# Kernel optimization log

Hardware: AMD Instinct MI355X
Metric: run time of the kernel (lower is better)

The kernel has to match this reference:

```python
import jax, jax.numpy as jnp
import numpy as np

B, L, D, N_ITEMS = 512, 100, 128, 100000
ALPHA = 0.3


def setup_inputs() -> dict:
    key = jax.random.key(0)
    ks = jax.random.split(key, 10)
    x = jax.random.randint(ks[0], (B, L), 0, N_ITEMS, dtype=jnp.int32)
    attn_mask = jnp.ones((B, L), dtype=bool)  # unused by forward (parity with torch signature)
    emb = jax.random.normal(ks[1], (N_ITEMS, D), dtype=jnp.float32) * 0.02
    emb = emb.at[0].set(0.0)  # padding_idx=0 row is zeros
    s = 1.0 / np.sqrt(D)
    W_in = jax.random.uniform(ks[2], (D, D), minval=-s, maxval=s, dtype=jnp.float32)
    W_out = jax.random.uniform(ks[3], (D, D), minval=-s, maxval=s, dtype=jnp.float32)
    w_ih = jax.random.uniform(ks[4], (3 * D, D), minval=-s, maxval=s, dtype=jnp.float32)
    w_hh = jax.random.uniform(ks[5], (3 * D, D), minval=-s, maxval=s, dtype=jnp.float32)
    b_ih = jax.random.uniform(ks[6], (3 * D,), minval=-s, maxval=s, dtype=jnp.float32)
    b_hh = jax.random.uniform(ks[7], (3 * D,), minval=-s, maxval=s, dtype=jnp.float32)
    sr = 1.0 / np.sqrt(3 * D)
    W_read = jax.random.uniform(ks[8], (D, 3 * D), minval=-sr, maxval=sr, dtype=jnp.float32)
    b_read = jax.random.uniform(ks[9], (D,), minval=-sr, maxval=sr, dtype=jnp.float32)
    return dict(x=x, attn_mask=attn_mask, emb=emb, W_in=W_in, W_out=W_out,
                w_ih=w_ih, w_hh=w_hh, b_ih=b_ih, b_hh=b_hh, W_read=W_read, b_read=b_read)


def _forward(x, emb, W_in, W_out, w_ih, w_hh, b_ih, b_hh, W_read, b_read):
    n_items, d = emb.shape
    seq_len = x.shape[1]
    BIG = n_items  # sentinel > any item id
    NEG = -1e9

    def per_sample(seq):
        valid = seq != 0
        cnt = valid.sum()
        # --- torch.unique(nonzero, return_inverse=True) via sort + dedup ---
        s = jnp.where(valid, seq, BIG)
        ss = jnp.sort(s)
        prev = jnp.concatenate([jnp.full((1,), -1, ss.dtype), ss[:-1]])
        is_first = (ss != prev) & (ss != BIG)
        n_nodes = is_first.sum()
        rank = jnp.cumsum(is_first) - 1
        nodes_s = jnp.full((seq_len,), BIG, ss.dtype).at[
            jnp.where(is_first, rank, seq_len)].set(ss, mode='drop')  # sorted unique ids, BIG-padded
        node_mask = jnp.arange(seq_len) < n_nodes
        nodes = jnp.where(node_mask, nodes_s, 0)  # pad slots -> item 0 (zero emb row)
        inv = jnp.searchsorted(nodes_s, s)  # inverse indices for valid positions
        # compact nonzero items preserving order (for consecutive-pair edges)
        pos = jnp.cumsum(valid) - 1
        cidx = jnp.where(valid, pos, seq_len)
        compact_inv = jnp.zeros((seq_len,), inv.dtype).at[cidx].set(inv, mode='drop')
        compact_seq = jnp.zeros((seq_len,), seq.dtype).at[cidx].set(seq, mode='drop')
        last_tok = compact_seq[jnp.maximum(cnt - 1, 0)]
        src, dst = compact_inv[:-1], compact_inv[1:]
        edge_mask = jnp.arange(seq_len - 1) < cnt - 1
        # --- message passing: index_add + degree normalize ---
        H0 = emb[nodes]  # [L, d]
        Hin = H0 @ W_in.T
        Hout = H0 @ W_out.T
        dst_safe = jnp.where(edge_mask, dst, seq_len)
        agg = jnp.zeros((seq_len, d), H0.dtype).at[dst_safe].add(
            jnp.where(edge_mask[:, None], Hout[src], 0.0), mode='drop')
        deg = jnp.zeros((seq_len,), H0.dtype).at[dst_safe].add(1.0, mode='drop')
        deg = jnp.maximum(deg, 1.0)
        xin = Hin + agg / deg[:, None]
        # --- GRUCell(xin, H0), torch gate order (r, z, n) ---
        gi = xin @ w_ih.T + b_ih
        gh = H0 @ w_hh.T + b_hh
        gi_r, gi_z, gi_n = jnp.split(gi, 3, axis=-1)
        gh_r, gh_z, gh_n = jnp.split(gh, 3, axis=-1)
        r = jax.nn.sigmoid(gi_r + gh_r)
        z = jax.nn.sigmoid(gi_z + gh_z)
        nct = jnp.tanh(gi_n + r * gh_n)
        H = (1.0 - z) * nct + z * H0
        H = jnp.where(node_mask[:, None], H, 0.0)  # drop padded node slots
        # --- attention readout anchored at last item ---
        li = jnp.clip(jnp.searchsorted(nodes_s, last_tok), 0, seq_len - 1)
        h_last = H[li]
        scores = jnp.where(node_mask, H @ h_last, NEG)
        att = jax.nn.softmax(scores)
        local = att @ H
        gvec = jnp.zeros((d,), H.dtype)  # cooc is None -> zeros_like(local)
        h_read = jnp.tanh(W_read @ jnp.concatenate([h_last, local, ALPHA * gvec]) + b_read)
        row = h_read @ emb.T  # tied output weights
        default = jnp.full((n_items,), NEG, row.dtype).at[0].set(0.0)
        return jnp.where(cnt >= 2, row, default)

    return jax.vmap(per_sample)(x)


def reference(x, attn_mask, emb, W_in, W_out, w_ih, w_hh, b_ih, b_hh, W_read, b_read):
    return _forward(x, emb, W_in, W_out, w_ih, w_hh, b_ih, b_hh, W_read, b_read)
```

## Files before the change

kernel.cpp:

```cpp
#include <hip/hip_runtime.h>
#include <math.h>

#define BATCH 512
#define SEQL  100
#define DIM   128
#define NITEMS 100000
#define NEGV  -1000000000.0f

#define OFF_WREADT 131072
#define OFF_HREAD  180224
#define OFF_DEG    245760
#define OFF_XIN    296960
#define OFF_HOUT   6850560
#define OFF_EPACK_F (OFF_XIN + 131072)
#define OFF_NODES_I 13404160
#define OFF_SRC_I   13455360
#define OFF_DST_I   13506048
#define OFF_INFO_I  13556736
#define OFF_WPACK_F 13558784

typedef __attribute__((ext_vector_type(8))) short bf16x8;
typedef __attribute__((ext_vector_type(4))) short s16x4;
typedef __attribute__((ext_vector_type(4))) float f32x4;

__device__ __forceinline__ unsigned short bf16_rne(float x) {
  unsigned int u = __float_as_uint(x);
  unsigned int r = u + 0x7FFFu + ((u >> 16) & 1u);
  return (unsigned short)(r >> 16);
}
__device__ __forceinline__ float bf16_to_f(unsigned short h) {
  return __uint_as_float(((unsigned int)h) << 16);
}

__global__ void k_prep(const float* __restrict__ w_ih, const float* __restrict__ w_hh,
                       const float* __restrict__ W_in, const float* __restrict__ W_out,
                       const float* __restrict__ W_read, float* __restrict__ ws,
                       unsigned short* __restrict__ wpack) {
  int idx = blockIdx.x * 256 + threadIdx.x;
  if (idx < 98304) {
    int mat = idx / 49152, rem = idx % 49152;
    int n = rem / 128, k = rem % 128;
    float v = (mat ? w_hh : w_ih)[rem];
    unsigned short hi = bf16_rne(v);
    unsigned short lo = bf16_rne(v - bf16_to_f(hi));
    int nt = n >> 4, nn = n & 15, c = k >> 5, quad = (k >> 3) & 3, j = k & 7;
    int lane = quad * 16 + nn;
    size_t base = ((size_t)((mat * 24 + nt) * 4 + c)) * 1024 + (size_t)lane * 8 + j;
    wpack[base] = hi;
    wpack[base + 512] = lo;
  }
  if (idx < 49152) {
    int i = idx / 384, jj = idx % 384;
    ws[OFF_WREADT + jj * 128 + i] = W_read[idx];
  }
  if (idx < 32768) {
    int mat = idx >> 14, rem = idx & 16383;
    int n = rem >> 7, k = rem & 127;
    float v = (mat ? W_out : W_in)[rem];
    unsigned short hi = bf16_rne(v);
    unsigned short lo = bf16_rne(v - bf16_to_f(hi));
    int nt = n >> 4, nn = n & 15, c = k >> 5, quad = (k >> 3) & 3, j = k & 7;
    int lane = quad * 16 + nn;
    size_t base = ((size_t)((mat * 8 + nt) * 4 + c)) * 1024 + (size_t)lane * 8 + j;
    unsigned short* wpack2 = (unsigned short*)ws;
    wpack2[base] = hi;
    wpack2[base + 512] = lo;
  }
}

__global__ void k_build(const int* __restrict__ x, int* __restrict__ nodes,
                        float* __restrict__ deg, int* __restrict__ esrc,
                        int* __restrict__ edst, int* __restrict__ info) {
  int b = blockIdx.x, tid = threadIdx.x;
  __shared__ int sseq[SEQL];
  __shared__ int sfo[SEQL];
  __shared__ unsigned char sisf[SEQL];
  __shared__ int srank[SEQL];
  __shared__ int spos[SEQL];
  __shared__ int scinv[SEQL];
  __shared__ float sdeg[SEQL];
  __shared__ int s_nn, s_cnt;

  if (tid < SEQL) sseq[tid] = x[b * SEQL + tid];
  __syncthreads();
  int t = (tid < SEQL) ? sseq[tid] : 0;
  bool valid = (tid < SEQL) && (t != 0);
  int f = tid;
  if (valid) {
    for (int j = 0; j < tid; ++j) {
      if (sseq[j] == t) { f = j; break; }
    }
  }
  if (tid < SEQL) {
    sfo[tid] = f;
    sisf[tid] = (valid && f == tid) ? 1 : 0;
    sdeg[tid] = 0.f;
  }
  __syncthreads();
  if (tid == 0) {
    int nn = 0, c = 0;
    for (int i = 0; i < SEQL; ++i) {
      srank[i] = nn; nn += sisf[i];
      spos[i] = c;  c += (sseq[i] != 0) ? 1 : 0;
    }
    s_nn = nn; s_cnt = c;
  }
  __syncthreads();
  int nn = s_nn, cnt = s_cnt;
  if (valid) scinv[spos[tid]] = srank[sfo[tid]];
  __syncthreads();
  if (tid < SEQL) {
    if (sisf[tid]) nodes[b * SEQL + srank[tid]] = t;
    if (tid >= nn) nodes[b * SEQL + tid] = 0;
  }
  __syncthreads();
  if (tid == 0) {
    int ec = (cnt >= 2) ? cnt - 1 : 0;
    for (int e = 0; e < ec; ++e) {
      int s = scinv[e], dnode = scinv[e + 1];
      esrc[b * 99 + e] = s;
      edst[b * 99 + e] = dnode;
      sdeg[dnode] += 1.f;
    }
    info[b * 4 + 0] = ec;
    info[b * 4 + 1] = (cnt >= 1) ? scinv[cnt - 1] : 0;
    info[b * 4 + 2] = (cnt >= 2) ? 1 : 0;
    info[b * 4 + 3] = nn;
  }
  __syncthreads();
  if (tid < SEQL) deg[b * SEQL + tid] = fmaxf(sdeg[tid], 1.f);
}

#define GPAD 136
__global__ __launch_bounds__(128) void k_gemm_inout(
    const float* __restrict__ emb, const unsigned short* __restrict__ wpack2,
    const int* __restrict__ nodes, float* __restrict__ xin, float* __restrict__ hout) {
  __shared__ unsigned short Hhi[32 * GPAD];
  __shared__ unsigned short Hlo[32 * GPAD];
  int tid = threadIdx.x;
  int rowbase = blockIdx.x * 32;
  const float4* emb4 = (const float4*)emb;
  for (int e = tid; e < 32 * 32; e += 128) {
    int r = e >> 5, c4 = e & 31;
    int tok = nodes[rowbase + r];
    float4 hv = emb4[(size_t)tok * 32 + c4];
    int base = r * GPAD + c4 * 4;
    float hs[4] = {hv.x, hv.y, hv.z, hv.w};
    #pragma unroll
    for (int q = 0; q < 4; ++q) {
      unsigned short hh = bf16_rne(hs[q]);
      Hhi[base + q] = hh;
      Hlo[base + q] = bf16_rne(hs[q] - bf16_to_f(hh));
    }
  }
  __syncthreads();
  int wave = tid >> 6, lane = tid & 63;
  int quad = lane >> 4, nIdx = lane & 15;
  int mrow = wave * 16 + nIdx;
  bf16x8 aH[4], aL[4];
  #pragma unroll
  for (int c = 0; c < 4; ++c) {
    int off = mrow * GPAD + c * 32 + quad * 8;
    aH[c] = *(const bf16x8*)&Hhi[off];
    aL[c] = *(const bf16x8*)&Hlo[off];
  }
  for (int t = 0; t < 8; ++t) {
    f32x4 accI = (f32x4){0.f, 0.f, 0.f, 0.f};
    f32x4 accO = (f32x4){0.f, 0.f, 0.f, 0.f};
    #pragma unroll
    for (int c = 0; c < 4; ++c) {
      size_t bi = ((size_t)((0 * 8 + t) * 4 + c)) * 1024 + (size_t)lane * 8;
      size_t bo = ((size_t)((1 * 8 + t) * 4 + c)) * 1024 + (size_t)lane * 8;
      bf16x8 BiH = *(const bf16x8*)&wpack2[bi];
      bf16x8 BiL = *(const bf16x8*)&wpack2[bi + 512];
      bf16x8 BoH = *(const bf16x8*)&wpack2[bo];
      bf16x8 BoL = *(const bf16x8*)&wpack2[bo + 512];
      accI = __builtin_amdgcn_mfma_f32_16x16x32_bf16(aH[c], BiH, accI, 0, 0, 0);
      accO = __builtin_amdgcn_mfma_f32_16x16x32_bf16(aH[c], BoH, accO, 0, 0, 0);
      accI = __builtin_amdgcn_mfma_f32_16x16x32_bf16(aL[c], BiH, accI, 0, 0, 0);
      accO = __builtin_amdgcn_mfma_f32_16x16x32_bf16(aL[c], BoH, accO, 0, 0, 0);
      accI = __builtin_amdgcn_mfma_f32_16x16x32_bf16(aH[c], BiL, accI, 0, 0, 0);
      accO = __builtin_amdgcn_mfma_f32_16x16x32_bf16(aH[c], BoL, accO, 0, 0, 0);
    }
    int j = t * 16 + nIdx;
    #pragma unroll
    for (int i = 0; i < 4; ++i) {
      size_t row = (size_t)(rowbase + wave * 16 + quad * 4 + i);
      xin[row * 128 + j]  = accI[i];
      hout[row * 128 + j] = accO[i];
    }
  }
}

__global__ void k_scatter(const float* __restrict__ hout, float* __restrict__ xin,
                          const float* __restrict__ deg, const int* __restrict__ esrc,
                          const int* __restrict__ edst, const int* __restrict__ info) {
  int b = blockIdx.x, k = threadIdx.x;
  __shared__ float agg[SEQL * DIM];
  for (int n = 0; n < SEQL; ++n) agg[n * DIM + k] = 0.f;
  int ec = info[b * 4 + 0];
  for (int e = 0; e < ec; ++e) {
    int s = esrc[b * 99 + e], dn = edst[b * 99 + e];
    agg[dn * DIM + k] += hout[((size_t)(b * SEQL + s)) * DIM + k];
  }
  for (int n = 0; n < SEQL; ++n) {
    float dg = deg[b * SEQL + n];
    size_t idx = ((size_t)(b * SEQL + n)) * DIM + k;
    xin[idx] += agg[n * DIM + k] / dg;
  }
}

__global__ __launch_bounds__(128) void k_gru(
    const float* __restrict__ emb, const int* __restrict__ nodes,
    const unsigned short* __restrict__ wpack, const float* __restrict__ xin,
    const float* __restrict__ b_ih, const float* __restrict__ b_hh,
    const int* __restrict__ info, float* __restrict__ Hbuf) {
  __shared__ unsigned short Xhi[32 * GPAD];
  __shared__ unsigned short Xlo[32 * GPAD];
  __shared__ unsigned short Hhi[32 * GPAD];
  __shared__ unsigned short Hlo[32 * GPAD];
  int tid = threadIdx.x;
  int rowbase = blockIdx.x * 32;
  const float4* emb4 = (const float4*)emb;
  const float4* xin4 = (const float4*)xin;
  for (int e = tid; e < 32 * 32; e += 128) {
    int r = e >> 5, c4 = e & 31;
    int row = rowbase + r;
    float4 xv = xin4[(size_t)row * 32 + c4];
    int tok = nodes[row];
    float4 hv = emb4[(size_t)tok * 32 + c4];
    int base = r * GPAD + c4 * 4;
    float xs[4] = {xv.x, xv.y, xv.z, xv.w};
    float hs[4] = {hv.x, hv.y, hv.z, hv.w};
    #pragma unroll
    for (int q = 0; q < 4; ++q) {
      unsigned short xh = bf16_rne(xs[q]);
      Xhi[base + q] = xh; Xlo[base + q] = bf16_rne(xs[q] - bf16_to_f(xh));
      unsigned short hh = bf16_rne(hs[q]);
      Hhi[base + q] = hh; Hlo[base + q] = bf16_rne(hs[q] - bf16_to_f(hh));
    }
  }
  __syncthreads();
  int wave = tid >> 6, lane = tid & 63;
  int quad = lane >> 4, nIdx = lane & 15;
  int mrow = wave * 16 + nIdx;
  bf16x8 aXh[4], aXl[4], aHh[4], aHl[4];
  #pragma unroll
  for (int c = 0; c < 4; ++c) {
    int off = mrow * GPAD + c * 32 + quad * 8;
    aXh[c] = *(const bf16x8*)&Xhi[off];
    aXl[c] = *(const bf16x8*)&Xlo[off];
    aHh[c] = *(const bf16x8*)&Hhi[off];
    aHl[c] = *(const bf16x8*)&Hlo[off];
  }
  int grows[4]; int zm[4];
  #pragma unroll
  for (int i = 0; i < 4; ++i) {
    int grow = rowbase + wave * 16 + quad * 4 + i;
    grows[i] = grow;
    int bs = grow / SEQL;
    int n = grow - bs * SEQL;
    zm[i] = (n < info[bs * 4 + 3]) ? 1 : 0;
  }

  for (int t = 0; t < 8; ++t) {
    f32x4 acc[3][2];
    #pragma unroll
    for (int g = 0; g < 3; ++g)
      #pragma unroll
      for (int m = 0; m < 2; ++m) acc[g][m] = (f32x4){0.f, 0.f, 0.f, 0.f};

    for (int c = 0; c < 4; ++c) {
      bf16x8 Bh[3][2], Bl[3][2];
      #pragma unroll
      for (int g = 0; g < 3; ++g) {
        int nt = g * 8 + t;
        #pragma unroll
        for (int m = 0; m < 2; ++m) {
          size_t bidx = (size_t)((m * 24 + nt) * 4 + c) * 1024 + (size_t)lane * 8;
          Bh[g][m] = *(const bf16x8*)&wpack[bidx];
          Bl[g][m] = *(const bf16x8*)&wpack[bidx + 512];
        }
      }
      #pragma unroll
      for (int g = 0; g < 3; ++g) {
        acc[g][0] = __builtin_amdgcn_mfma_f32_16x16x32_bf16(aXh[c], Bh[g][0], acc[g][0], 0, 0, 0);
        acc[g][1] = __builtin_amdgcn_mfma_f32_16x16x32_bf16(aHh[c], Bh[g][1], acc[g][1], 0, 0, 0);
      }
      #pragma unroll
      for (int g = 0; g < 3; ++g) {
        acc[g][0] = __builtin_amdgcn_mfma_f32_16x16x32_bf16(aXh[c], Bl[g][0], acc[g][0], 0, 0, 0);
        acc[g][1] = __builtin_amdgcn_mfma_f32_16x16x32_bf16(aHh[c], Bl[g][1], acc[g][1], 0, 0, 0);
      }
      #pragma unroll
      for (int g = 0; g < 3; ++g) {
        acc[g][0] = __builtin_amdgcn_mfma_f32_16x16x32_bf16(aXl[c], Bh[g][0], acc[g][0], 0, 0, 0);
        acc[g][1] = __builtin_amdgcn_mfma_f32_16x16x32_bf16(aHl[c], Bh[g][1], acc[g][1], 0, 0, 0);
      }
    }
    int j = t * 16 + nIdx;
    float biR = b_ih[j],       bhR = b_hh[j];
    float biZ = b_ih[128 + j], bhZ = b_hh[128 + j];
    float biN = b_ih[256 + j], bhN = b_hh[256 + j];
    #pragma unroll
    for (int i = 0; i < 4; ++i) {
      float gr = acc[0][0][i] + biR + acc[0][1][i] + bhR;
      float gz = acc[1][0][i] + biZ + acc[1][1][i] + bhZ;
      float r = 1.f / (1.f + expf(-gr));
      float z = 1.f / (1.f + expf(-gz));
      float nct = tanhf(acc[2][0][i] + biN + r * (acc[2][1][i] + bhN));
      int lrow = wave * 16 + quad * 4 + i;
      float h0 = bf16_to_f(Hhi[lrow * GPAD + j]) + bf16_to_f(Hlo[lrow * GPAD + j]);
      float h = (1.f - z) * nct + z * h0;
      if (!zm[i]) h = 0.f;
      Hbuf[(size_t)grows[i] * 128 + j] = h;
    }
  }
}

#define HLS 129
__global__ void k_attn(const float* __restrict__ Hbuf, const float* __restrict__ ws,
                       const float* __restrict__ b_read, const int* __restrict__ info,
                       float* __restrict__ hread) {
  int b = blockIdx.x, tid = threadIdx.x;
  __shared__ float Hl[SEQL * HLS];
  __shared__ float sc[128];
  __shared__ float hl[128];
  __shared__ float att[SEQL];
  __shared__ float loc[128];
  __shared__ float redm[2], reds[2];
  int nn = info[b * 4 + 3], li = info[b * 4 + 1];
  for (int e = tid; e < SEQL * 128; e += 128) {
    int r = e >> 7, k = e & 127;
    Hl[r * HLS + k] = Hbuf[((size_t)(b * SEQL + r)) * DIM + k];
  }
  __syncthreads();
  hl[tid] = Hl[li * HLS + tid];
  __syncthreads();
  float scr = NEGV;
  if (tid < nn) {
    float s = 0.f;
    for (int k = 0; k < 128; ++k) s += Hl[tid * HLS + k] * hl[k];
    scr = s;
  }
  sc[tid] = scr;
  __syncthreads();
  float m = sc[tid];
  #pragma unroll
  for (int o = 32; o >= 1; o >>= 1) m = fmaxf(m, __shfl_xor(m, o, 64));
  if ((tid & 63) == 0) redm[tid >> 6] = m;
  __syncthreads();
  m = fmaxf(redm[0], redm[1]);
  float e = (tid < SEQL) ? expf(sc[tid] - m) : 0.f;
  float s = e;
  #pragma unroll
  for (int o = 32; o >= 1; o >>= 1) s += __shfl_xor(s, o, 64);
  if ((tid & 63) == 0) reds[tid >> 6] = s;
  __syncthreads();
  float inv = 1.f / (reds[0] + reds[1]);
  if (tid < SEQL) att[tid] = e * inv;
  __syncthreads();
  float lv = 0.f;
  for (int n = 0; n < SEQL; ++n) lv = fmaf(att[n], Hl[n * HLS + tid], lv);
  loc[tid] = lv;
  __syncthreads();
  const float* WrT = ws + OFF_WREADT;
  float acc = b_read[tid];
  for (int j = 0; j < 128; ++j) acc = fmaf(WrT[j * 128 + tid], hl[j], acc);
  for (int j = 0; j < 128; ++j) acc = fmaf(WrT[(128 + j) * 128 + tid], loc[j], acc);
  hread[b * 128 + tid] = tanhf(acc);
}

__global__ __launch_bounds__(256) void k_packA(
    const float* __restrict__ hread, unsigned short* __restrict__ apack) {
  int idx = blockIdx.x * 256 + threadIdx.x;
  if (idx >= 8192) return;
  int lane = idx & 63;
  int kc = (idx >> 6) & 3;
  int mt = idx >> 8;
  int quad = lane >> 4, rr = lane & 15;
  int row = mt * 16 + rr;
  int kbase = kc * 32 + quad * 8;
  const float4* hr4 = (const float4*)(hread + row * 128 + kbase);
  float4 v0 = hr4[0], v1 = hr4[1];
  float vs[8] = {v0.x, v0.y, v0.z, v0.w, v1.x, v1.y, v1.z, v1.w};
  bf16x8 hi, lo;
  #pragma unroll
  for (int j = 0; j < 8; ++j) {
    unsigned short h = bf16_rne(vs[j]);
    hi[j] = (short)h;
    lo[j] = (short)bf16_rne(vs[j] - bf16_to_f(h));
  }
  size_t base = ((size_t)(mt * 4 + kc) * 2) * 512 + (size_t)lane * 8;
  *(bf16x8*)&apack[base] = hi;
  *(bf16x8*)&apack[base + 512] = lo;
}

__global__ __launch_bounds__(256) void k_epack(
    const float* __restrict__ emb, unsigned short* __restrict__ epack) {
  int idx = blockIdx.x * 256 + threadIdx.x;
  int lane = idx & 63;
  int kc = (idx >> 6) & 3;
  int it = idx >> 8;
  int quad = lane >> 4, rr = lane & 15;
  int row = it * 16 + rr;
  int kbase = kc * 32 + quad * 8;
  float4 v0 = {0.f, 0.f, 0.f, 0.f}, v1 = {0.f, 0.f, 0.f, 0.f};
  if (row < NITEMS) {
    const float4* p = (const float4*)(emb + (size_t)row * 128 + kbase);
    v0 = p[0]; v1 = p[1];
  }
  float vs[8] = {v0.x, v0.y, v0.z, v0.w, v1.x, v1.y, v1.z, v1.w};
  bf16x8 hi, lo;
  #pragma unroll
  for (int j = 0; j < 8; ++j) {
    unsigned short h = bf16_rne(vs[j]);
    hi[j] = (short)h;
    lo[j] = (short)bf16_rne(vs[j] - bf16_to_f(h));
  }
  size_t base = ((size_t)(it * 4 + kc) * 2) * 512 + (size_t)lane * 8;
  *(bf16x8*)&epack[base] = hi;
  *(bf16x8*)&epack[base + 512] = lo;
}

__global__ __launch_bounds__(256) void k_out(
    const unsigned short* __restrict__ epack, const unsigned short* __restrict__ apack,
    const int* __restrict__ info, float* __restrict__ out) {
  int tid = threadIdx.x;
  int wave = tid >> 6, lane = tid & 63;
  int quad = lane >> 4, nIdx = lane & 15;
  int b0   = blockIdx.x * 128;
  int itt0 = blockIdx.y * 4;
  int btg0 = blockIdx.x * 8 + wave * 2;

  bf16x8 bh[2][4], bl[2][4];
  #pragma unroll
  for (int m2 = 0; m2 < 2; ++m2)
    #pragma unroll
    for (int kc = 0; kc < 4; ++kc) {
      size_t base = ((size_t)((btg0 + m2) * 4 + kc) * 2) * 512 + (size_t)lane * 8;
      bh[m2][kc] = *(const bf16x8*)&apack[base];
      bl[m2][kc] = *(const bf16x8*)&apack[base + 512];
    }

  f32x4 acc[4][2];
  #pragma unroll
  for (int it = 0; it < 4; ++it)
    #pragma unroll
    for (int m2 = 0; m2 < 2; ++m2) acc[it][m2] = (f32x4){0.f, 0.f, 0.f, 0.f};

  #pragma unroll
  for (int it = 0; it < 4; ++it) {
    #pragma unroll
    for (int kc = 0; kc < 4; ++kc) {
      size_t abase = ((size_t)((itt0 + it) * 4 + kc) * 2) * 512 + (size_t)lane * 8;
      bf16x8 Ah = *(const bf16x8*)&epack[abase];
      bf16x8 Al = *(const bf16x8*)&epack[abase + 512];
      acc[it][0] = __builtin_amdgcn_mfma_f32_16x16x32_bf16(Ah, bh[0][kc], acc[it][0], 0, 0, 0);
      acc[it][1] = __builtin_amdgcn_mfma_f32_16x16x32_bf16(Ah, bh[1][kc], acc[it][1], 0, 0, 0);
      acc[it][0] = __builtin_amdgcn_mfma_f32_16x16x32_bf16(Al, bh[0][kc], acc[it][0], 0, 0, 0);
      acc[it][1] = __builtin_amdgcn_mfma_f32_16x16x32_bf16(Al, bh[1][kc], acc[it][1], 0, 0, 0);
      acc[it][0] = __builtin_amdgcn_mfma_f32_16x16x32_bf16(Ah, bl[0][kc], acc[it][0], 0, 0, 0);
      acc[it][1] = __builtin_amdgcn_mfma_f32_16x16x32_bf16(Ah, bl[1][kc], acc[it][1], 0, 0, 0);
    }
  }

  #pragma unroll
  for (int m2 = 0; m2 < 2; ++m2) {
    int b = b0 + (wave * 2 + m2) * 16 + nIdx;
    int flag = info[b * 4 + 2];
    #pragma unroll
    for (int it = 0; it < 4; ++it) {
      int ib = (itt0 + it) * 16 + quad * 4;
      if (ib < NITEMS) {
        float4 v;
        if (flag) {
          v.x = acc[it][m2][0]; v.y = acc[it][m2][1];
          v.z = acc[it][m2][2]; v.w = acc[it][m2][3];
        } else {
          v.x = (ib == 0) ? 0.f : NEGV; v.y = NEGV; v.z = NEGV; v.w = NEGV;
        }
        *(float4*)&out[(size_t)b * NITEMS + ib] = v;
      }
    }
  }
}

extern "C" void kernel_launch(void* const* d_in, const int* in_sizes, int n_in,
                              void* d_out, int out_size, void* d_ws, size_t ws_size,
                              hipStream_t stream) {
  const int*   x      = (const int*)d_in[0];
  const float* emb    = (const float*)d_in[2];
  const float* W_in   = (const float*)d_in[3];
  const float* W_out  = (const float*)d_in[4];
  const float* w_ih   = (const float*)d_in[5];
  const float* w_hh   = (const float*)d_in[6];
  const float* b_ih   = (const float*)d_in[7];
  const float* b_hh   = (const float*)d_in[8];
  const float* W_read = (const float*)d_in[9];
  const float* b_read = (const float*)d_in[10];
  float* ws  = (float*)d_ws;
  int*   wsi = (int*)d_ws;
  unsigned short* wpack  = (unsigned short*)(ws + OFF_WPACK_F);
  unsigned short* wpack2 = (unsigned short*)ws;
  unsigned short* apack  = (unsigned short*)(ws + OFF_XIN);
  unsigned short* epack  = (unsigned short*)(ws + OFF_EPACK_F);
  float* out = (float*)d_out;

  k_prep<<<384, 256, 0, stream>>>(w_ih, w_hh, W_in, W_out, W_read, ws, wpack);
  k_build<<<BATCH, 128, 0, stream>>>(x, wsi + OFF_NODES_I, ws + OFF_DEG,
                                     wsi + OFF_SRC_I, wsi + OFF_DST_I, wsi + OFF_INFO_I);
  k_gemm_inout<<<1600, 128, 0, stream>>>(emb, wpack2, wsi + OFF_NODES_I,
                                         ws + OFF_XIN, ws + OFF_HOUT);
  k_scatter<<<BATCH, 128, 0, stream>>>(ws + OFF_HOUT, ws + OFF_XIN, ws + OFF_DEG,
                                       wsi + OFF_SRC_I, wsi + OFF_DST_I, wsi + OFF_INFO_I);
  k_gru<<<1600, 128, 0, stream>>>(emb, wsi + OFF_NODES_I, wpack, ws + OFF_XIN,
                                  b_ih, b_hh, wsi + OFF_INFO_I, ws + OFF_HOUT);
  k_attn<<<BATCH, 128, 0, stream>>>(ws + OFF_HOUT, ws, b_read, wsi + OFF_INFO_I,
                                    ws + OFF_HREAD);
  k_epack<<<6252, 256, 0, stream>>>(emb, epack);
  k_packA<<<32, 256, 0, stream>>>(ws + OFF_HREAD, apack);
  k_out<<<dim3(4, 1563), 256, 0, stream>>>(epack, apack, wsi + OFF_INFO_I, out);
}
```

Baseline: 473.5 us.

## Parallelize graph build and scatter, fuse A-packing into attention readout

Replaces the single-thread serial prefix scans and edge loop in k_build with per-thread scans and parallel edge writes, and moves degree counting into k_scatter via shared-memory atomics. k_scatter now uses 256 threads, parallelizes over edges×dims with LDS atomics, and applies the degree normalization in a fused vectorized pass. The separate k_packA launch is removed by having k_attn write the bf16 hi/lo packed output directly. This targets serial latency and launch overhead in the small kernels. The trade-off is float atomic ordering nondeterminism in aggregation and O(n) per-thread scans.

```diff
diff --git a/kernel.cpp b/kernel.cpp
--- a/kernel.cpp
+++ b/kernel.cpp
@@ -8,8 +8,6 @@
 #define NEGV  -1000000000.0f
 
 #define OFF_WREADT 131072
-#define OFF_HREAD  180224
-#define OFF_DEG    245760
 #define OFF_XIN    296960
 #define OFF_HOUT   6850560
 #define OFF_EPACK_F (OFF_XIN + 131072)
@@ -69,66 +67,52 @@
 }
 
 __global__ void k_build(const int* __restrict__ x, int* __restrict__ nodes,
-                        float* __restrict__ deg, int* __restrict__ esrc,
-                        int* __restrict__ edst, int* __restrict__ info) {
+                        int* __restrict__ esrc, int* __restrict__ edst,
+                        int* __restrict__ info) {
   int b = blockIdx.x, tid = threadIdx.x;
   __shared__ int sseq[SEQL];
-  __shared__ int sfo[SEQL];
   __shared__ unsigned char sisf[SEQL];
   __shared__ int srank[SEQL];
-  __shared__ int spos[SEQL];
   __shared__ int scinv[SEQL];
-  __shared__ float sdeg[SEQL];
+  __shared__ int snodes[SEQL];
   __shared__ int s_nn, s_cnt;
-
-  if (tid < SEQL) sseq[tid] = x[b * SEQL + tid];
+  if (tid < SEQL) { sseq[tid] = x[b * SEQL + tid]; snodes[tid] = 0; }
   __syncthreads();
   int t = (tid < SEQL) ? sseq[tid] : 0;
   bool valid = (tid < SEQL) && (t != 0);
   int f = tid;
   if (valid) {
-    for (int j = 0; j < tid; ++j) {
-      if (sseq[j] == t) { f = j; break; }
-    }
-  }
+    for (int j = 0; j < tid; ++j) if (sseq[j] == t) { f = j; break; }
+  }
+  int isf = (valid && f == tid) ? 1 : 0;
+  if (tid < SEQL) sisf[tid] = (unsigned char)isf;
+  __syncthreads();
+  int rank = 0, pos = 0;
   if (tid < SEQL) {
-    sfo[tid] = f;
-    sisf[tid] = (valid && f == tid) ? 1 : 0;
-    sdeg[tid] = 0.f;
-  }
-  __syncthreads();
+    for (int i = 0; i < tid; ++i) {
+      rank += sisf[i];
+      pos += (sseq[i] != 0) ? 1 : 0;
+    }
+    srank[tid] = rank;
+    if (tid == SEQL - 1) { s_nn = rank + isf; s_cnt = pos + (valid ? 1 : 0); }
+  }
+  __syncthreads();
+  if (valid) scinv[pos] = srank[f];
+  if (isf) snodes[rank] = t;
+  __syncthreads();
+  int cnt = s_cnt;
+  int ec = (cnt >= 2) ? cnt - 1 : 0;
+  if (tid < ec) {
+    esrc[b * 99 + tid] = scinv[tid];
+    edst[b * 99 + tid] = scinv[tid + 1];
+  }
   if (tid == 0) {
-    int nn = 0, c = 0;
-    for (int i = 0; i < SEQL; ++i) {
-      srank[i] = nn; nn += sisf[i];
-      spos[i] = c;  c += (sseq[i] != 0) ? 1 : 0;
-    }
-    s_nn = nn; s_cnt = c;
-  }
-  __syncthreads();
-  int nn = s_nn, cnt = s_cnt;
-  if (valid) scinv[spos[tid]] = srank[sfo[tid]];
-  __syncthreads();
-  if (tid < SEQL) {
-    if (sisf[tid]) nodes[b * SEQL + srank[tid]] = t;
-    if (tid >= nn) nodes[b * SEQL + tid] = 0;
-  }
-  __syncthreads();
-  if (tid == 0) {
-    int ec = (cnt >= 2) ? cnt - 1 : 0;
-    for (int e = 0; e < ec; ++e) {
-      int s = scinv[e], dnode = scinv[e + 1];
-      esrc[b * 99 + e] = s;
-      edst[b * 99 + e] = dnode;
-      sdeg[dnode] += 1.f;
-    }
     info[b * 4 + 0] = ec;
     info[b * 4 + 1] = (cnt >= 1) ? scinv[cnt - 1] : 0;
     info[b * 4 + 2] = (cnt >= 2) ? 1 : 0;
-    info[b * 4 + 3] = nn;
-  }
-  __syncthreads();
-  if (tid < SEQL) deg[b * SEQL + tid] = fmaxf(sdeg[tid], 1.f);
+    info[b * 4 + 3] = s_nn;
+  }
+  if (tid < SEQL) nodes[b * SEQL + tid] = snodes[tid];
 }
 
 #define GPAD 136
@@ -192,21 +176,29 @@
   }
 }
 
-__global__ void k_scatter(const float* __restrict__ hout, float* __restrict__ xin,
-                          const float* __restrict__ deg, const int* __restrict__ esrc,
-                          const int* __restrict__ edst, const int* __restrict__ info) {
-  int b = blockIdx.x, k = threadIdx.x;
+__global__ __launch_bounds__(256) void k_scatter(
+    const float* __restrict__ hout, float* __restrict__ xin,
+    const int* __restrict__ esrc, const int* __restrict__ edst,
+    const int* __restrict__ info) {
   __shared__ float agg[SEQL * DIM];
-  for (int n = 0; n < SEQL; ++n) agg[n * DIM + k] = 0.f;
+  __shared__ float sdeg[SEQL];
+  int b = blockIdx.x, tid = threadIdx.x;
+  float4* a4 = (float4*)agg;
+  for (int e = tid; e < SEQL * 32; e += 256) a4[e] = (float4){0.f, 0.f, 0.f, 0.f};
+  if (tid < SEQL) sdeg[tid] = 0.f;
+  __syncthreads();
   int ec = info[b * 4 + 0];
-  for (int e = 0; e < ec; ++e) {
+  if (tid < ec) atomicAdd(&sdeg[edst[b * 99 + tid]], 1.f);
+  for (int idx = tid; idx < ec * DIM; idx += 256) {
+    int e = idx >> 7, k = idx & 127;
     int s = esrc[b * 99 + e], dn = edst[b * 99 + e];
-    agg[dn * DIM + k] += hout[((size_t)(b * SEQL + s)) * DIM + k];
-  }
-  for (int n = 0; n < SEQL; ++n) {
-    float dg = deg[b * SEQL + n];
-    size_t idx = ((size_t)(b * SEQL + n)) * DIM + k;
-    xin[idx] += agg[n * DIM + k] / dg;
+    atomicAdd(&agg[dn * DIM + k], hout[((size_t)(b * SEQL + s)) * DIM + k]);
+  }
+  __syncthreads();
+  for (int idx = tid; idx < SEQL * DIM; idx += 256) {
+    int n = idx >> 7;
+    size_t g = ((size_t)b * SEQL) * DIM + idx;
+    xin[g] += agg[idx] * (1.f / fmaxf(sdeg[n], 1.f));
   }
 }
 
@@ -319,9 +311,9 @@
 }
 
 #define HLS 129
-__global__ void k_attn(const float* __restrict__ Hbuf, const float* __restrict__ ws,
+__global__ void k_attn(const float* __restrict__ Hbuf, const float* __restrict__ WrT,
                        const float* __restrict__ b_read, const int* __restrict__ info,
-                       float* __restrict__ hread) {
+                       unsigned short* __restrict__ apack) {
   int b = blockIdx.x, tid = threadIdx.x;
   __shared__ float Hl[SEQL * HLS];
   __shared__ float sc[128];
@@ -364,36 +356,17 @@
   for (int n = 0; n < SEQL; ++n) lv = fmaf(att[n], Hl[n * HLS + tid], lv);
   loc[tid] = lv;
   __syncthreads();
-  const float* WrT = ws + OFF_WREADT;
   float acc = b_read[tid];
   for (int j = 0; j < 128; ++j) acc = fmaf(WrT[j * 128 + tid], hl[j], acc);
   for (int j = 0; j < 128; ++j) acc = fmaf(WrT[(128 + j) * 128 + tid], loc[j], acc);
-  hread[b * 128 + tid] = tanhf(acc);
-}
-
-__global__ __launch_bounds__(256) void k_packA(
-    const float* __restrict__ hread, unsigned short* __restrict__ apack) {
-  int idx = blockIdx.x * 256 + threadIdx.x;
-  if (idx >= 8192) return;
-  int lane = idx & 63;
-  int kc = (idx >> 6) & 3;
-  int mt = idx >> 8;
-  int quad = lane >> 4, rr = lane & 15;
-  int row = mt * 16 + rr;
-  int kbase = kc * 32 + quad * 8;
-  const float4* hr4 = (const float4*)(hread + row * 128 + kbase);
-  float4 v0 = hr4[0], v1 = hr4[1];
-  float vs[8] = {v0.x, v0.y, v0.z, v0.w, v1.x, v1.y, v1.z, v1.w};
-  bf16x8 hi, lo;
-  #pragma unroll
-  for (int j = 0; j < 8; ++j) {
-    unsigned short h = bf16_rne(vs[j]);
-    hi[j] = (short)h;
-    lo[j] = (short)bf16_rne(vs[j] - bf16_to_f(h));
-  }
-  size_t base = ((size_t)(mt * 4 + kc) * 2) * 512 + (size_t)lane * 8;
-  *(bf16x8*)&apack[base] = hi;
-  *(bf16x8*)&apack[base + 512] = lo;
+  float hr = tanhf(acc);
+  int mt = b >> 4, rr = b & 15;
+  int kc = tid >> 5, q2 = (tid >> 3) & 3, j2 = tid & 7;
+  unsigned short hi = bf16_rne(hr);
+  unsigned short lo = bf16_rne(hr - bf16_to_f(hi));
+  size_t base = ((size_t)(mt * 4 + kc) * 2) * 512 + (size_t)(q2 * 16 + rr) * 8 + j2;
+  apack[base] = hi;
+  apack[base + 512] = lo;
 }
 
 __global__ __launch_bounds__(256) void k_epack(
@@ -508,17 +481,16 @@
   float* out = (float*)d_out;
 
   k_prep<<<384, 256, 0, stream>>>(w_ih, w_hh, W_in, W_out, W_read, ws, wpack);
-  k_build<<<BATCH, 128, 0, stream>>>(x, wsi + OFF_NODES_I, ws + OFF_DEG,
+  k_build<<<BATCH, 128, 0, stream>>>(x, wsi + OFF_NODES_I,
                                      wsi + OFF_SRC_I, wsi + OFF_DST_I, wsi + OFF_INFO_I);
   k_gemm_inout<<<1600, 128, 0, stream>>>(emb, wpack2, wsi + OFF_NODES_I,
                                          ws + OFF_XIN, ws + OFF_HOUT);
-  k_scatter<<<BATCH, 128, 0, stream>>>(ws + OFF_HOUT, ws + OFF_XIN, ws + OFF_DEG,
+  k_scatter<<<BATCH, 256, 0, stream>>>(ws + OFF_HOUT, ws + OFF_XIN,
                                        wsi + OFF_SRC_I, wsi + OFF_DST_I, wsi + OFF_INFO_I);
   k_gru<<<1600, 128, 0, stream>>>(emb, wsi + OFF_NODES_I, wpack, ws + OFF_XIN,
                                   b_ih, b_hh, wsi + OFF_INFO_I, ws + OFF_HOUT);
-  k_attn<<<BATCH, 128, 0, stream>>>(ws + OFF_HOUT, ws, b_read, wsi + OFF_INFO_I,
-                                    ws + OFF_HREAD);
+  k_attn<<<BATCH, 128, 0, stream>>>(ws + OFF_HOUT, ws + OFF_WREADT, b_read,
+                                    wsi + OFF_INFO_I, apack);
   k_epack<<<6252, 256, 0, stream>>>(emb, epack);
-  k_packA<<<32, 256, 0, stream>>>(ws + OFF_HREAD, apack);
   k_out<<<dim3(4, 1563), 256, 0, stream>>>(epack, apack, wsi + OFF_INFO_I, out);
 }
```

Result: slower. 484.9 us (+2.4%).
